# Kernel tuning notes

Measured on AMD Instinct MI355X. Metric: run time of the kernel, lower is better.

Reference implementation:

```python
import jax, jax.numpy as jnp
import numpy as np

DIM, M, K = 768, 48, 256
MK = M * K            # 12288
H = MK // 2           # 6144
MID = int(0.75 * MK)  # 9216
B = 2048
MIN_DIST_FACTOR = 10.0
LN_EPS = 1e-5


def setup_inputs() -> dict:
    key = jax.random.key(0)
    ks = jax.random.split(key, 18)
    s = 0.02  # keep exp(sigma_logits) tame
    return {
        "x": jax.random.normal(ks[0], (B, DIM), jnp.float32),
        "codebook": jax.random.normal(ks[1], (M, K, DIM // M), jnp.float32),
        "rot1": jnp.eye(DIM) + s * jax.random.normal(ks[2], (DIM, DIM), jnp.float32),
        "ln_g": jnp.ones((DIM,), jnp.float32),
        "ln_b": jnp.zeros((DIM,), jnp.float32),
        "l1_w": s * jax.random.normal(ks[3], (MID, DIM), jnp.float32),
        "l1_b": jnp.zeros((MID,), jnp.float32),
        "mu_w": s * jax.random.normal(ks[4], (H, MID), jnp.float32),
        "mu_b": jnp.zeros((H,), jnp.float32),
        "sig_w": s * jax.random.normal(ks[5], (H, MID), jnp.float32),
        "sig_b": jnp.zeros((H,), jnp.float32),
        "rot2": jnp.eye(H) + s * jax.random.normal(ks[6], (H, H), jnp.float32),
        "l2_w": s * jax.random.normal(ks[7], (MK, H), jnp.float32),
        "l2_b": jnp.zeros((MK,), jnp.float32),
        "interp_param": jax.random.normal(ks[8], (1,), jnp.float32),
        "vae_noise": jax.random.normal(ks[9], (B, H), jnp.float32),
        "gumbel_noise": -jnp.log(-jnp.log(
            jax.random.uniform(ks[10], (B, M, K), jnp.float32, 1e-10, 1.0))),
    }


def _layernorm(x, g, b):
    mu = jnp.mean(x, axis=-1, keepdims=True)
    var = jnp.mean((x - mu) ** 2, axis=-1, keepdims=True)
    return (x - mu) * jax.lax.rsqrt(var + LN_EPS) * g + b


def reference(x, codebook, rot1, ln_g, ln_b, l1_w, l1_b, mu_w, mu_b,
              sig_w, sig_b, rot2, l2_w, l2_b, interp_param,
              vae_noise, gumbel_noise):
    x_rot = x @ rot1.T                                   # [B, DIM]
    xn = _layernorm(x_rot, ln_g, ln_b)
    h1 = jax.nn.relu(xn @ l1_w.T + l1_b)                 # [B, MID]
    mu = h1 @ mu_w.T + mu_b                              # [B, H]
    sigma = jnp.exp(h1 @ sig_w.T + sig_b)                # [B, H]
    z = mu + sigma * vae_noise                           # reparameterized sample
    h = jnp.tanh(z)
    h_rot = h @ rot2.T                                   # [B, H]
    a = jax.nn.relu(h_rot @ l2_w.T + l2_b)               # [B, MK]
    a_r = a.reshape(-1, M, K)                            # [B, M, K]
    # PQ distances: [B, M, 1, d] vs [1, M, K, d] -> [B, M, K]
    d = DIM // M
    xs = x_rot.reshape(-1, M, 1, d)
    cs = codebook.reshape(1, M, K, d)
    dist = jnp.sum((cs - xs) ** 2, axis=-1)
    min_dist = jax.nn.one_hot(jnp.argmin(dist, axis=-1), K, dtype=jnp.float32)
    interp = jax.nn.sigmoid(interp_param[0])
    logits = (1.0 - interp) * a_r + interp * MIN_DIST_FACTOR * min_dist
    # hard gumbel-softmax, tau=1
    y_soft = jax.nn.softmax(logits + gumbel_noise, axis=-1)
    y_hard = jax.nn.one_hot(jnp.argmax(y_soft, axis=-1), K, dtype=y_soft.dtype)
    s = y_hard - jax.lax.stop_gradient(y_soft) + y_soft
    return s
```

## Files before the change

kernel.cpp:

```cpp
#include <hip/hip_runtime.h>
#include <cstddef>
#include <cstdint>

constexpr int kDIM = 768;
constexpr int kM   = 48;
constexpr int kK   = 256;
constexpr int kB   = 2048;
constexpr int kMID = 9216;
constexpr int kH   = 6144;
constexpr int kMK  = 12288;

using bf8v  = __attribute__((ext_vector_type(8))) short;
using f32x4 = __attribute__((ext_vector_type(4))) float;
using s8v   = __attribute__((ext_vector_type(8))) short;

#define GLL16(SRC, DST) __builtin_amdgcn_global_load_lds( \
    (const __attribute__((address_space(1))) void*)(SRC), \
    (__attribute__((address_space(3))) void*)(DST), 16, 0, 0)

template<bool HASBIAS, int EPI, typename OUT_T>
__global__ __launch_bounds__(256)
void gemm_nt_acc64(const float* __restrict__ A, const float* __restrict__ W,
                   const float* __restrict__ bias, OUT_T* C,
                   const float* zslog, const float* __restrict__ znoise,
                   int N, int Kd)
{
  __shared__ float As[16][132];
  __shared__ float Bs[16][132];
  const int tid  = (int)threadIdx.x;
  const int row0 = (int)blockIdx.y * 128;
  const int col0 = (int)blockIdx.x * 128;
  const int ty = tid >> 4, tx = tid & 15;
  const int i0 = ty * 8, j0 = tx * 8;
  const int fi1 = tid >> 2;
  const int fi2 = fi1 + 64;
  const int kc  = (tid & 3) * 4;

  const float* Ap1 = A + (size_t)(row0 + fi1) * Kd + kc;
  const float* Ap2 = A + (size_t)(row0 + fi2) * Kd + kc;
  const float* Wp1 = W + (size_t)(col0 + fi1) * Kd + kc;
  const float* Wp2 = W + (size_t)(col0 + fi2) * Kd + kc;

  double acc[8][8];
#pragma unroll
  for (int r = 0; r < 8; ++r)
#pragma unroll
    for (int c = 0; c < 8; ++c) acc[r][c] = 0.0;

  for (int kt = 0; kt < Kd; kt += 16) {
    const float4 a1 = *(const float4*)(Ap1 + kt);
    const float4 a2 = *(const float4*)(Ap2 + kt);
    const float4 b1 = *(const float4*)(Wp1 + kt);
    const float4 b2 = *(const float4*)(Wp2 + kt);
    As[kc + 0][fi1] = a1.x; As[kc + 1][fi1] = a1.y; As[kc + 2][fi1] = a1.z; As[kc + 3][fi1] = a1.w;
    As[kc + 0][fi2] = a2.x; As[kc + 1][fi2] = a2.y; As[kc + 2][fi2] = a2.z; As[kc + 3][fi2] = a2.w;
    Bs[kc + 0][fi1] = b1.x; Bs[kc + 1][fi1] = b1.y; Bs[kc + 2][fi1] = b1.z; Bs[kc + 3][fi1] = b1.w;
    Bs[kc + 0][fi2] = b2.x; Bs[kc + 1][fi2] = b2.y; Bs[kc + 2][fi2] = b2.z; Bs[kc + 3][fi2] = b2.w;
    __syncthreads();
#pragma unroll
    for (int kk = 0; kk < 16; ++kk) {
      const float4 av0 = *(const float4*)&As[kk][i0];
      const float4 av1 = *(const float4*)&As[kk][i0 + 4];
      const float4 bv0 = *(const float4*)&Bs[kk][j0];
      const float4 bv1 = *(const float4*)&Bs[kk][j0 + 4];
      const float ar[8] = {av0.x, av0.y, av0.z, av0.w, av1.x, av1.y, av1.z, av1.w};
      const float br[8] = {bv0.x, bv0.y, bv0.z, bv0.w, bv1.x, bv1.y, bv1.z, bv1.w};
      double bd[8];
#pragma unroll
      for (int c = 0; c < 8; ++c) bd[c] = (double)br[c];
#pragma unroll
      for (int r = 0; r < 8; ++r) {
        const double ad = (double)ar[r];
#pragma unroll
        for (int c = 0; c < 8; ++c)
          acc[r][c] = fma(ad, bd[c], acc[r][c]);
      }
    }
    __syncthreads();
  }

  double bvv[8];
#pragma unroll
  for (int c = 0; c < 8; ++c) bvv[c] = 0.0;
  if (HASBIAS) {
#pragma unroll
    for (int c = 0; c < 8; ++c) bvv[c] = (double)bias[col0 + j0 + c];
  }

#pragma unroll
  for (int r = 0; r < 8; ++r) {
    const size_t gbase = (size_t)(row0 + i0 + r) * N + col0 + j0;
    double o[8];
#pragma unroll
    for (int c = 0; c < 8; ++c) {
      double v = acc[r][c];
      if (HASBIAS) v += bvv[c];
      if (EPI == 1) v = fmax(v, 0.0);
      if (EPI == 2) {
        const double sg = exp((double)zslog[gbase + c]);
        v = tanh(v + sg * (double)znoise[gbase + c]);
      }
      o[c] = v;
    }
    if constexpr (sizeof(OUT_T) == 4) {
      float* dst = (float*)C + gbase;
      ((float4*)dst)[0] = make_float4((float)o[0], (float)o[1], (float)o[2], (float)o[3]);
      ((float4*)dst)[1] = make_float4((float)o[4], (float)o[5], (float)o[6], (float)o[7]);
    } else {
      double* dst = (double*)C + gbase;
#pragma unroll
      for (int c = 0; c < 8; ++c) dst[c] = o[c];
    }
  }
}

__device__ __forceinline__ unsigned short bf16rn(float f) {
  const unsigned u = __float_as_uint(f);
  return (unsigned short)((u + 0x7FFFu + ((u >> 16) & 1u)) >> 16);
}

__global__ __launch_bounds__(256)
void split3_k(const float* __restrict__ in, short* __restrict__ out, size_t n)
{
  const size_t i = ((size_t)blockIdx.x * 256 + threadIdx.x) * 8;
  const float4 v0 = *(const float4*)(in + i);
  const float4 v1 = *(const float4*)(in + i + 4);
  const float f[8] = {v0.x, v0.y, v0.z, v0.w, v1.x, v1.y, v1.z, v1.w};
  s8v o1, o2, o3;
#pragma unroll
  for (int j = 0; j < 8; ++j) {
    const unsigned short b1 = bf16rn(f[j]);
    const float r1 = f[j] - __uint_as_float((unsigned)b1 << 16);
    const unsigned short b2 = bf16rn(r1);
    const float r2 = r1 - __uint_as_float((unsigned)b2 << 16);
    const unsigned short b3 = bf16rn(r2);
    o1[j] = (short)b1; o2[j] = (short)b2; o3[j] = (short)b3;
  }
  *(s8v*)(out + i)         = o1;
  *(s8v*)(out + n + i)     = o2;
  *(s8v*)(out + 2 * n + i) = o3;
}

template<bool HASBIAS, bool RELU>
__global__ __launch_bounds__(256, 3)
void gemm3_bf16(const short* __restrict__ A3, const short* __restrict__ W3,
                const float* __restrict__ bias, float* __restrict__ C,
                int N, int Kd, int nbx)
{
  __shared__ short lds[6][4096];
  short* smem = &lds[0][0];
  const char* smemc = (const char*)smem;

  int wg = (int)blockIdx.x;
  const int nwg = (int)gridDim.x;
  if ((nwg & 7) == 0) { const int q = nwg >> 3; wg = (wg & 7) * q + (wg >> 3); }
  const int nby = kB / 128;
  const int by = wg % nby, bx = wg / nby;
  const int row0 = by * 128, col0 = bx * 128;

  const int tid = (int)threadIdx.x;
  const int l = tid & 63, w = tid >> 6;
  const int wr = (w & 1) * 64, wc = (w >> 1) * 64;

  const size_t planeAB = (size_t)2048 * Kd * 2;
  const size_t planeWB = (size_t)N * Kd * 2;
  const char* A3b = (const char*)A3;
  const char* W3b = (const char*)W3;

  const int su = 2 * w;
  const int r0 = su * 16 + (l >> 2), r1 = r0 + 16;
  const int qsw = (((l & 3) ^ ((l >> 3) & 3)) << 4);
  const size_t offA0 = (size_t)(row0 + r0) * Kd * 2 + qsw;
  const size_t offA1 = (size_t)(row0 + r1) * Kd * 2 + qsw;
  const size_t offW0 = (size_t)(col0 + r0) * Kd * 2 + qsw;
  const size_t offW1 = (size_t)(col0 + r1) * Kd * 2 + qsw;
  short* dA0 = smem + (su + 0) * 512;
  short* dA1 = smem + (su + 1) * 512;

  int aoff[3][4], boff[3][4];
#pragma unroll
  for (int p = 0; p < 3; ++p) {
#pragma unroll
    for (int t = 0; t < 4; ++t) {
      const int Ra = wr + t * 16 + (l & 15);
      aoff[p][t] = p * 8192 + Ra * 64 + ((((l >> 4)) ^ ((Ra >> 1) & 3)) << 4);
      const int Rb = wc + t * 16 + (l & 15);
      boff[p][t] = (3 + p) * 8192 + Rb * 64 + ((((l >> 4)) ^ ((Rb >> 1) & 3)) << 4);
    }
  }

  f32x4 acc[4][4];
#pragma unroll
  for (int i = 0; i < 4; ++i)
#pragma unroll
    for (int j = 0; j < 4; ++j) acc[i][j] = f32x4{0.f, 0.f, 0.f, 0.f};

  for (int kt = 0; kt < Kd; kt += 32) {
    const size_t kb = (size_t)kt * 2;
#pragma unroll
    for (int t = 0; t < 3; ++t) {
      GLL16(A3b + t * planeAB + offA0 + kb, dA0 + t * 4096);
      GLL16(A3b + t * planeAB + offA1 + kb, dA1 + t * 4096);
    }
#pragma unroll
    for (int t = 0; t < 3; ++t) {
      GLL16(W3b + t * planeWB + offW0 + kb, dA0 + (3 + t) * 4096);
      GLL16(W3b + t * planeWB + offW1 + kb, dA1 + (3 + t) * 4096);
    }
    __syncthreads();

    bf8v af[3][4], bf_[3][4];
#pragma unroll
    for (int p = 0; p < 3; ++p)
#pragma unroll
      for (int t = 0; t < 4; ++t) {
        af[p][t]  = *(const bf8v*)(smemc + aoff[p][t]);
        bf_[p][t] = *(const bf8v*)(smemc + boff[p][t]);
      }
#pragma unroll
    for (int tr = 0; tr < 4; ++tr)
#pragma unroll
      for (int tc = 0; tc < 4; ++tc) {
        f32x4 c = acc[tr][tc];
        c = __builtin_amdgcn_mfma_f32_16x16x32_bf16(af[0][tr], bf_[0][tc], c, 0, 0, 0);
        c = __builtin_amdgcn_mfma_f32_16x16x32_bf16(af[0][tr], bf_[1][tc], c, 0, 0, 0);
        c = __builtin_amdgcn_mfma_f32_16x16x32_bf16(af[1][tr], bf_[0][tc], c, 0, 0, 0);
        c = __builtin_amdgcn_mfma_f32_16x16x32_bf16(af[0][tr], bf_[2][tc], c, 0, 0, 0);
        c = __builtin_amdgcn_mfma_f32_16x16x32_bf16(af[2][tr], bf_[0][tc], c, 0, 0, 0);
        c = __builtin_amdgcn_mfma_f32_16x16x32_bf16(af[1][tr], bf_[1][tc], c, 0, 0, 0);
        acc[tr][tc] = c;
      }
    __syncthreads();
  }

#pragma unroll
  for (int tc = 0; tc < 4; ++tc) {
    const int colg = col0 + wc + tc * 16 + (l & 15);
    float bv = 0.f;
    if (HASBIAS) bv = bias[colg];
#pragma unroll
    for (int tr = 0; tr < 4; ++tr) {
      const int rowg0 = row0 + wr + tr * 16 + ((l >> 4) << 2);
#pragma unroll
      for (int g = 0; g < 4; ++g) {
        float v = acc[tr][tc][g];
        if (HASBIAS) v += bv;
        if (RELU)    v = fmaxf(v, 0.f);
        C[(size_t)(rowg0 + g) * N + colg] = v;
      }
    }
  }
}

__global__ __launch_bounds__(256)
void layernorm_k(const double* __restrict__ in, const float* __restrict__ g,
                 const float* __restrict__ b, float* __restrict__ out)
{
  const int row = (int)blockIdx.x;
  const int tid = (int)threadIdx.x;
  const double* x = in + (size_t)row * kDIM;
  const double v0 = x[tid], v1 = x[tid + 256], v2 = x[tid + 512];
  __shared__ double red[8];
  double s = v0 + v1 + v2;
#pragma unroll
  for (int off = 32; off; off >>= 1) s += __shfl_xor(s, off);
  if ((tid & 63) == 0) red[tid >> 6] = s;
  __syncthreads();
  const double mean = (red[0] + red[1] + red[2] + red[3]) * (1.0 / 768.0);
  const double d0 = v0 - mean, d1 = v1 - mean, d2 = v2 - mean;
  double q = d0 * d0 + d1 * d1 + d2 * d2;
#pragma unroll
  for (int off = 32; off; off >>= 1) q += __shfl_xor(q, off);
  if ((tid & 63) == 0) red[4 + (tid >> 6)] = q;
  __syncthreads();
  const double var = (red[4] + red[5] + red[6] + red[7]) * (1.0 / 768.0);
  const double rs = 1.0 / sqrt(var + 1e-5);
  float* y = out + (size_t)row * kDIM;
  y[tid]       = (float)(d0 * rs * (double)g[tid]       + (double)b[tid]);
  y[tid + 256] = (float)(d1 * rs * (double)g[tid + 256] + (double)b[tid + 256]);
  y[tid + 512] = (float)(d2 * rs * (double)g[tid + 512] + (double)b[tid + 512]);
}

__global__ __launch_bounds__(256)
void zh_k(const float* __restrict__ mu, float* slog_h, const float* __restrict__ noise)
{
  const size_t i = (size_t)blockIdx.x * 256 + threadIdx.x;
  const double z = (double)mu[i] + exp((double)slog_h[i]) * (double)noise[i];
  slog_h[i] = (float)tanh(z);
}

__global__ __launch_bounds__(256)
void mindist_k(const double* __restrict__ xrot, const float* __restrict__ cb,
               int* __restrict__ minidx)
{
  const int wid  = (int)blockIdx.x * 4 + ((int)threadIdx.x >> 6);
  const int lane = (int)threadIdx.x & 63;
  const int bi = wid / kM, mi = wid % kM;
  const double* xv = xrot + (size_t)bi * kDIM + mi * 16;
  double xs[16];
#pragma unroll
  for (int d = 0; d < 16; ++d) xs[d] = xv[d];
  const float* cm = cb + (size_t)mi * (kK * 16);
  double best = 1e300; int bidx = 0;
#pragma unroll
  for (int j = 0; j < 4; ++j) {
    const int k = lane * 4 + j;
    const float* ck = cm + k * 16;
    double s = 0.0;
#pragma unroll
    for (int d = 0; d < 16; ++d) {
      const double t = (double)ck[d] - xs[d];
      s = fma(t, t, s);
    }
    if (s < best) { best = s; bidx = k; }
  }
#pragma unroll
  for (int off = 32; off; off >>= 1) {
    const double ob = __shfl_xor(best, off);
    const int    oi = __shfl_xor(bidx, off);
    if (ob < best || (ob == best && oi < bidx)) { best = ob; bidx = oi; }
  }
  if (lane == 0) minidx[wid] = bidx;
}

__global__ __launch_bounds__(256)
void finalize_k(float* a, const float* __restrict__ gumbel,
                const int* __restrict__ minidx, const float* __restrict__ interp_param)
{
  const int wid  = (int)blockIdx.x * 4 + ((int)threadIdx.x >> 6);
  const int lane = (int)threadIdx.x & 63;
  const double interp = 1.0 / (1.0 + exp(-(double)interp_param[0]));
  const double w = 1.0 - interp;
  const double bonus = interp * 10.0;
  const int mi = minidx[wid];
  const size_t base = (size_t)wid * 256 + lane * 4;
  const float4 av = *(const float4*)&a[base];
  const float4 gv = *(const float4*)&gumbel[base];
  const int k0 = lane * 4;
  double lg[4] = {w * (double)av.x + (double)gv.x,
                  w * (double)av.y + (double)gv.y,
                  w * (double)av.z + (double)gv.z,
                  w * (double)av.w + (double)gv.w};
#pragma unroll
  for (int j = 0; j < 4; ++j)
    if (k0 + j == mi) lg[j] += bonus;

  double best = -1e300; int bk = 0;
#pragma unroll
  for (int j = 0; j < 4; ++j)
    if (lg[j] > best) { best = lg[j]; bk = k0 + j; }
#pragma unroll
  for (int off = 32; off; off >>= 1) {
    const double ob = __shfl_xor(best, off);
    const int    oi = __shfl_xor(bk, off);
    if (ob > best || (ob == best && oi < bk)) { best = ob; bk = oi; }
  }
  float4 o;
  o.x = (k0 + 0 == bk) ? 1.f : 0.f;
  o.y = (k0 + 1 == bk) ? 1.f : 0.f;
  o.z = (k0 + 2 == bk) ? 1.f : 0.f;
  o.w = (k0 + 3 == bk) ? 1.f : 0.f;
  *(float4*)&a[base] = o;
}

extern "C" void kernel_launch(void* const* d_in, const int* in_sizes, int n_in,
                              void* d_out, int out_size, void* d_ws, size_t ws_size,
                              hipStream_t stream)
{
  const float* x      = (const float*)d_in[0];
  const float* cb     = (const float*)d_in[1];
  const float* rot1   = (const float*)d_in[2];
  const float* ln_g   = (const float*)d_in[3];
  const float* ln_b   = (const float*)d_in[4];
  const float* l1_w   = (const float*)d_in[5];
  const float* l1_b   = (const float*)d_in[6];
  const float* mu_w   = (const float*)d_in[7];
  const float* mu_b   = (const float*)d_in[8];
  const float* sig_w  = (const float*)d_in[9];
  const float* sig_b  = (const float*)d_in[10];
  const float* rot2   = (const float*)d_in[11];
  const float* l2_w   = (const float*)d_in[12];
  const float* l2_b   = (const float*)d_in[13];
  const float* interp = (const float*)d_in[14];
  const float* noise  = (const float*)d_in[15];
  const float* gumb   = (const float*)d_in[16];

  const dim3 blk(256);
  float* aout = (float*)d_out;

  const size_t nXrot = (size_t)kB * kDIM;
  const size_t nH1   = (size_t)kB * kMID;
  const size_t nHH   = (size_t)kB * kH;
  const size_t NEED  = nXrot * 8 + nXrot * 4 + nH1 * 4 + nHH * 4 + nHH * 4
                     + nH1 * 3 * 2 + (size_t)kMK * kH * 3 * 2 + (size_t)kB * kM * 4;

  if (ws_size >= NEED) {
    char* p = (char*)d_ws;
    double* x_rotd = (double*)p;              p += nXrot * 8;
    float*  xn     = (float*)p;               p += nXrot * 4;
    float*  h1     = (float*)p;               p += nH1 * 4;
    float*  mu     = (float*)p;               p += nHH * 4;
    float*  slog   = (float*)p;               p += nHH * 4;
    short*  As3    = (short*)p;               p += nH1 * 3 * 2;
    short*  Ws3    = (short*)p;               p += (size_t)kMK * kH * 3 * 2;
    int*    midx   = (int*)p;

    gemm_nt_acc64<false, 0, double><<<dim3(kDIM / 128, kB / 128), blk, 0, stream>>>(
        x, rot1, nullptr, x_rotd, nullptr, nullptr, kDIM, kDIM);
    layernorm_k<<<dim3(kB), blk, 0, stream>>>(x_rotd, ln_g, ln_b, xn);
    mindist_k<<<dim3(kB * kM / 4), blk, 0, stream>>>(x_rotd, cb, midx);

    split3_k<<<dim3((unsigned)(nXrot / 2048)), blk, 0, stream>>>(xn, As3, nXrot);
    split3_k<<<dim3((unsigned)((size_t)kMID * kDIM / 2048)), blk, 0, stream>>>(l1_w, Ws3, (size_t)kMID * kDIM);
    gemm3_bf16<true, true><<<dim3(kMID / 128 * (kB / 128)), blk, 0, stream>>>(
        As3, Ws3, l1_b, h1, kMID, kDIM, kMID / 128);

    split3_k<<<dim3((unsigned)(nH1 / 2048)), blk, 0, stream>>>(h1, As3, nH1);
    split3_k<<<dim3((unsigned)((size_t)kH * kMID / 2048)), blk, 0, stream>>>(mu_w, Ws3, (size_t)kH * kMID);
    gemm3_bf16<true, false><<<dim3(kH / 128 * (kB / 128)), blk, 0, stream>>>(
        As3, Ws3, mu_b, mu, kH, kMID, kH / 128);
    split3_k<<<dim3((unsigned)((size_t)kH * kMID / 2048)), blk, 0, stream>>>(sig_w, Ws3, (size_t)kH * kMID);
    gemm3_bf16<true, false><<<dim3(kH / 128 * (kB / 128)), blk, 0, stream>>>(
        As3, Ws3, sig_b, slog, kH, kMID, kH / 128);

    zh_k<<<dim3((unsigned)(nHH / 256)), blk, 0, stream>>>(mu, slog, noise);

    split3_k<<<dim3((unsigned)(nHH / 2048)), blk, 0, stream>>>(slog, As3, nHH);
    split3_k<<<dim3((unsigned)((size_t)kH * kH / 2048)), blk, 0, stream>>>(rot2, Ws3, (size_t)kH * kH);
    gemm3_bf16<false, false><<<dim3(kH / 128 * (kB / 128)), blk, 0, stream>>>(
        As3, Ws3, nullptr, h1, kH, kH, kH / 128);

    split3_k<<<dim3((unsigned)(nHH / 2048)), blk, 0, stream>>>(h1, As3, nHH);
    split3_k<<<dim3((unsigned)((size_t)kMK * kH / 2048)), blk, 0, stream>>>(l2_w, Ws3, (size_t)kMK * kH);
    gemm3_bf16<true, true><<<dim3(kMK / 128 * (kB / 128)), blk, 0, stream>>>(
        As3, Ws3, l2_b, aout, kMK, kH, kMK / 128);

    finalize_k<<<dim3(kB * kM / 4), blk, 0, stream>>>(aout, gumb, midx, interp);
    return;
  }

  char* wsb    = (char*)d_ws;
  double* x_rotd = (double*)wsb;
  float*  xn     = (float*)(wsb + (size_t)kB * kDIM * 8);
  float*  h1     = xn   + (size_t)kB * kDIM;
  float*  slog   = h1   + (size_t)kB * kMID;
  int*    midx   = (int*)(slog + (size_t)kB * kH);
  float*  hrot   = h1;

  gemm_nt_acc64<false, 0, double><<<dim3(kDIM / 128, kB / 128), blk, 0, stream>>>(
      x, rot1, nullptr, x_rotd, nullptr, nullptr, kDIM, kDIM);
  layernorm_k<<<dim3(kB), blk, 0, stream>>>(x_rotd, ln_g, ln_b, xn);
  mindist_k<<<dim3(kB * kM / 4), blk, 0, stream>>>(x_rotd, cb, midx);
  gemm_nt_acc64<true, 1, float><<<dim3(kMID / 128, kB / 128), blk, 0, stream>>>(
      xn, l1_w, l1_b, h1, nullptr, nullptr, kMID, kDIM);
  gemm_nt_acc64<true, 0, float><<<dim3(kH / 128, kB / 128), blk, 0, stream>>>(
      h1, sig_w, sig_b, slog, nullptr, nullptr, kH, kMID);
  gemm_nt_acc64<true, 2, float><<<dim3(kH / 128, kB / 128), blk, 0, stream>>>(
      h1, mu_w, mu_b, slog, slog, noise, kH, kMID);
  gemm_nt_acc64<false, 0, float><<<dim3(kH / 128, kB / 128), blk, 0, stream>>>(
      slog, rot2, nullptr, hrot, nullptr, nullptr, kH, kH);
  gemm_nt_acc64<true, 1, float><<<dim3(kMK / 128, kB / 128), blk, 0, stream>>>(
      hrot, l2_w, l2_b, aout, nullptr, nullptr, kMK, kH);
  finalize_k<<<dim3(kB * kM / 4), blk, 0, stream>>>(aout, gumb, midx, interp);
}
```

Measured before the change: 6.000 ms.

## Fuse bf16 triple-split and reparameterization into GEMM and layernorm epilogues

After: 6.320 ms. +5.3%, slower.

```diff
diff --git a/kernel.cpp b/kernel.cpp
--- a/kernel.cpp
+++ b/kernel.cpp
@@ -17,6 +17,11 @@
 #define GLL16(SRC, DST) __builtin_amdgcn_global_load_lds( \
     (const __attribute__((address_space(1))) void*)(SRC), \
     (__attribute__((address_space(3))) void*)(DST), 16, 0, 0)
+
+__device__ __forceinline__ unsigned short bf16rn(float f) {
+  const unsigned u = __float_as_uint(f);
+  return (unsigned short)((u + 0x7FFFu + ((u >> 16) & 1u)) >> 16);
+}
 
 template<bool HASBIAS, int EPI, typename OUT_T>
 __global__ __launch_bounds__(256)
@@ -114,11 +119,6 @@
   }
 }
 
-__device__ __forceinline__ unsigned short bf16rn(float f) {
-  const unsigned u = __float_as_uint(f);
-  return (unsigned short)((u + 0x7FFFu + ((u >> 16) & 1u)) >> 16);
-}
-
 __global__ __launch_bounds__(256)
 void split3_k(const float* __restrict__ in, short* __restrict__ out, size_t n)
 {
@@ -141,11 +141,12 @@
   *(s8v*)(out + 2 * n + i) = o3;
 }
 
-template<bool HASBIAS, bool RELU>
+template<bool HASBIAS, int EPI>
 __global__ __launch_bounds__(256, 3)
 void gemm3_bf16(const short* __restrict__ A3, const short* __restrict__ W3,
-                const float* __restrict__ bias, float* __restrict__ C,
-                int N, int Kd, int nbx)
+                const float* __restrict__ bias, void* C,
+                const float* __restrict__ zslog, const float* __restrict__ znoise,
+                int N, int Kd, size_t planeC)
 {
   __shared__ short lds[6][4096];
   short* smem = &lds[0][0];
@@ -243,18 +244,74 @@
       const int rowg0 = row0 + wr + tr * 16 + ((l >> 4) << 2);
 #pragma unroll
       for (int g = 0; g < 4; ++g) {
+        const size_t idx = (size_t)(rowg0 + g) * N + colg;
         float v = acc[tr][tc][g];
         if (HASBIAS) v += bv;
-        if (RELU)    v = fmaxf(v, 0.f);
-        C[(size_t)(rowg0 + g) * N + colg] = v;
+        if (EPI == 1 || EPI == 2) v = fmaxf(v, 0.f);
+        if (EPI == 3) {
+          const double z = (double)v +
+                           exp((double)zslog[idx]) * (double)znoise[idx];
+          v = (float)tanh(z);
+        }
+        if (EPI <= 1) {
+          ((float*)C)[idx] = v;
+        } else {
+          short* P = (short*)C;
+          const unsigned short b1 = bf16rn(v);
+          const float q1 = v - __uint_as_float((unsigned)b1 << 16);
+          const unsigned short b2 = bf16rn(q1);
+          const float q2 = q1 - __uint_as_float((unsigned)b2 << 16);
+          const unsigned short b3 = bf16rn(q2);
+          P[idx]              = (short)b1;
+          P[planeC + idx]     = (short)b2;
+          P[2 * planeC + idx] = (short)b3;
+        }
       }
     }
   }
 }
 
 __global__ __launch_bounds__(256)
-void layernorm_k(const double* __restrict__ in, const float* __restrict__ g,
-                 const float* __restrict__ b, float* __restrict__ out)
+void layernorm_sp_k(const double* __restrict__ in, const float* __restrict__ g,
+                    const float* __restrict__ b, short* __restrict__ outP, size_t nP)
+{
+  const int row = (int)blockIdx.x;
+  const int tid = (int)threadIdx.x;
+  const double* x = in + (size_t)row * kDIM;
+  const double v0 = x[tid], v1 = x[tid + 256], v2 = x[tid + 512];
+  __shared__ double red[8];
+  double s = v0 + v1 + v2;
+#pragma unroll
+  for (int off = 32; off; off >>= 1) s += __shfl_xor(s, off);
+  if ((tid & 63) == 0) red[tid >> 6] = s;
+  __syncthreads();
+  const double mean = (red[0] + red[1] + red[2] + red[3]) * (1.0 / 768.0);
+  const double d0 = v0 - mean, d1 = v1 - mean, d2 = v2 - mean;
+  double q = d0 * d0 + d1 * d1 + d2 * d2;
+#pragma unroll
+  for (int off = 32; off; off >>= 1) q += __shfl_xor(q, off);
+  if ((tid & 63) == 0) red[4 + (tid >> 6)] = q;
+  __syncthreads();
+  const double var = (red[4] + red[5] + red[6] + red[7]) * (1.0 / 768.0);
+  const double rs = 1.0 / sqrt(var + 1e-5);
+  const double dd[3] = {d0, d1, d2};
+#pragma unroll
+  for (int j = 0; j < 3; ++j) {
+    const int c = tid + j * 256;
+    const float y = (float)(dd[j] * rs * (double)g[c] + (double)b[c]);
+    const size_t idx = (size_t)row * kDIM + c;
+    const unsigned short b1 = bf16rn(y);
+    const float r1 = y - __uint_as_float((unsigned)b1 << 16);
+    const unsigned short b2 = bf16rn(r1);
+    const float r2 = r1 - __uint_as_float((unsigned)b2 << 16);
+    const unsigned short b3 = bf16rn(r2);
+    outP[idx] = (short)b1; outP[nP + idx] = (short)b2; outP[2 * nP + idx] = (short)b3;
+  }
+}
+
+__global__ __launch_bounds__(256)
+void layernorm_f32_k(const double* __restrict__ in, const float* __restrict__ g,
+                     const float* __restrict__ b, float* __restrict__ out)
 {
   const int row = (int)blockIdx.x;
   const int tid = (int)threadIdx.x;
@@ -279,14 +336,6 @@
   y[tid]       = (float)(d0 * rs * (double)g[tid]       + (double)b[tid]);
   y[tid + 256] = (float)(d1 * rs * (double)g[tid + 256] + (double)b[tid + 256]);
   y[tid + 512] = (float)(d2 * rs * (double)g[tid + 512] + (double)b[tid + 512]);
-}
-
-__global__ __launch_bounds__(256)
-void zh_k(const float* __restrict__ mu, float* slog_h, const float* __restrict__ noise)
-{
-  const size_t i = (size_t)blockIdx.x * 256 + threadIdx.x;
-  const double z = (double)mu[i] + exp((double)slog_h[i]) * (double)noise[i];
-  slog_h[i] = (float)tanh(z);
 }
 
 __global__ __launch_bounds__(256)
@@ -391,49 +440,49 @@
   const size_t nXrot = (size_t)kB * kDIM;
   const size_t nH1   = (size_t)kB * kMID;
   const size_t nHH   = (size_t)kB * kH;
-  const size_t NEED  = nXrot * 8 + nXrot * 4 + nH1 * 4 + nHH * 4 + nHH * 4
-                     + nH1 * 3 * 2 + (size_t)kMK * kH * 3 * 2 + (size_t)kB * kM * 4;
+  const size_t NEED  = nXrot * 8 + nXrot * 3 * 2 + nHH * 4 + nH1 * 3 * 2
+                     + nHH * 3 * 2 + (size_t)kMK * kH * 3 * 2 + (size_t)kB * kM * 4;
 
   if (ws_size >= NEED) {
     char* p = (char*)d_ws;
     double* x_rotd = (double*)p;              p += nXrot * 8;
-    float*  xn     = (float*)p;               p += nXrot * 4;
-    float*  h1     = (float*)p;               p += nH1 * 4;
-    float*  mu     = (float*)p;               p += nHH * 4;
+    short*  xnP    = (short*)p;               p += nXrot * 3 * 2;
     float*  slog   = (float*)p;               p += nHH * 4;
-    short*  As3    = (short*)p;               p += nH1 * 3 * 2;
+    short*  h1P    = (short*)p;               p += nH1 * 3 * 2;
+    short*  hP     = (short*)p;               p += nHH * 3 * 2;
     short*  Ws3    = (short*)p;               p += (size_t)kMK * kH * 3 * 2;
     int*    midx   = (int*)p;
+    short*  hrotP  = h1P;
 
     gemm_nt_acc64<false, 0, double><<<dim3(kDIM / 128, kB / 128), blk, 0, stream>>>(
         x, rot1, nullptr, x_rotd, nullptr, nullptr, kDIM, kDIM);
-    layernorm_k<<<dim3(kB), blk, 0, stream>>>(x_rotd, ln_g, ln_b, xn);
+    layernorm_sp_k<<<dim3(kB), blk, 0, stream>>>(x_rotd, ln_g, ln_b, xnP, nXrot);
     mindist_k<<<dim3(kB * kM / 4), blk, 0, stream>>>(x_rotd, cb, midx);
 
-    split3_k<<<dim3((unsigned)(nXrot / 2048)), blk, 0, stream>>>(xn, As3, nXrot);
-    split3_k<<<dim3((unsigned)((size_t)kMID * kDIM / 2048)), blk, 0, stream>>>(l1_w, Ws3, (size_t)kMID * kDIM);
-    gemm3_bf16<true, true><<<dim3(kMID / 128 * (kB / 128)), blk, 0, stream>>>(
-        As3, Ws3, l1_b, h1, kMID, kDIM, kMID / 128);
-
-    split3_k<<<dim3((unsigned)(nH1 / 2048)), blk, 0, stream>>>(h1, As3, nH1);
-    split3_k<<<dim3((unsigned)((size_t)kH * kMID / 2048)), blk, 0, stream>>>(mu_w, Ws3, (size_t)kH * kMID);
-    gemm3_bf16<true, false><<<dim3(kH / 128 * (kB / 128)), blk, 0, stream>>>(
-        As3, Ws3, mu_b, mu, kH, kMID, kH / 128);
-    split3_k<<<dim3((unsigned)((size_t)kH * kMID / 2048)), blk, 0, stream>>>(sig_w, Ws3, (size_t)kH * kMID);
-    gemm3_bf16<true, false><<<dim3(kH / 128 * (kB / 128)), blk, 0, stream>>>(
-        As3, Ws3, sig_b, slog, kH, kMID, kH / 128);
-
-    zh_k<<<dim3((unsigned)(nHH / 256)), blk, 0, stream>>>(mu, slog, noise);
-
-    split3_k<<<dim3((unsigned)(nHH / 2048)), blk, 0, stream>>>(slog, As3, nHH);
-    split3_k<<<dim3((unsigned)((size_t)kH * kH / 2048)), blk, 0, stream>>>(rot2, Ws3, (size_t)kH * kH);
-    gemm3_bf16<false, false><<<dim3(kH / 128 * (kB / 128)), blk, 0, stream>>>(
-        As3, Ws3, nullptr, h1, kH, kH, kH / 128);
-
-    split3_k<<<dim3((unsigned)(nHH / 2048)), blk, 0, stream>>>(h1, As3, nHH);
-    split3_k<<<dim3((unsigned)((size_t)kMK * kH / 2048)), blk, 0, stream>>>(l2_w, Ws3, (size_t)kMK * kH);
-    gemm3_bf16<true, true><<<dim3(kMK / 128 * (kB / 128)), blk, 0, stream>>>(
-        As3, Ws3, l2_b, aout, kMK, kH, kMK / 128);
+    split3_k<<<dim3((unsigned)((size_t)kMID * kDIM / 2048)), blk, 0, stream>>>(
+        l1_w, Ws3, (size_t)kMID * kDIM);
+    gemm3_bf16<true, 2><<<dim3(kMID / 128 * (kB / 128)), blk, 0, stream>>>(
+        xnP, Ws3, l1_b, h1P, nullptr, nullptr, kMID, kDIM, nH1);
+
+    split3_k<<<dim3((unsigned)((size_t)kH * kMID / 2048)), blk, 0, stream>>>(
+        sig_w, Ws3, (size_t)kH * kMID);
+    gemm3_bf16<true, 0><<<dim3(kH / 128 * (kB / 128)), blk, 0, stream>>>(
+        h1P, Ws3, sig_b, slog, nullptr, nullptr, kH, kMID, 0);
+
+    split3_k<<<dim3((unsigned)((size_t)kH * kMID / 2048)), blk, 0, stream>>>(
+        mu_w, Ws3, (size_t)kH * kMID);
+    gemm3_bf16<true, 3><<<dim3(kH / 128 * (kB / 128)), blk, 0, stream>>>(
+        h1P, Ws3, mu_b, hP, slog, noise, kH, kMID, nHH);
+
+    split3_k<<<dim3((unsigned)((size_t)kH * kH / 2048)), blk, 0, stream>>>(
+        rot2, Ws3, (size_t)kH * kH);
+    gemm3_bf16<false, 4><<<dim3(kH / 128 * (kB / 128)), blk, 0, stream>>>(
+        hP, Ws3, nullptr, hrotP, nullptr, nullptr, kH, kH, nHH);
+
+    split3_k<<<dim3((unsigned)((size_t)kMK * kH / 2048)), blk, 0, stream>>>(
+        l2_w, Ws3, (size_t)kMK * kH);
+    gemm3_bf16<true, 1><<<dim3(kMK / 128 * (kB / 128)), blk, 0, stream>>>(
+        hrotP, Ws3, l2_b, aout, nullptr, nullptr, kMK, kH, 0);
 
     finalize_k<<<dim3(kB * kM / 4), blk, 0, stream>>>(aout, gumb, midx, interp);
     return;
@@ -449,7 +498,7 @@
 
   gemm_nt_acc64<false, 0, double><<<dim3(kDIM / 128, kB / 128), blk, 0, stream>>>(
       x, rot1, nullptr, x_rotd, nullptr, nullptr, kDIM, kDIM);
-  layernorm_k<<<dim3(kB), blk, 0, stream>>>(x_rotd, ln_g, ln_b, xn);
+  layernorm_f32_k<<<dim3(kB), blk, 0, stream>>>(x_rotd, ln_g, ln_b, xn);
   mindist_k<<<dim3(kB * kM / 4), blk, 0, stream>>>(x_rotd, cb, midx);
   gemm_nt_acc64<true, 1, float><<<dim3(kMID / 128, kB / 128), blk, 0, stream>>>(
       xn, l1_w, l1_b, h1, nullptr, nullptr, kMID, kDIM);
```
